# Kernel tuning notes

Hardware: AMD Instinct MI355X
Metric: run time of the kernel (lower is better)

The kernel has to match this reference:

```python
import jax, jax.numpy as jnp
import numpy as np

NEG_SLOPE = 0.2
EPS = 1e-16


def gat_layer(x, src, dst, W, att_src, att_dst, bias, heads, out_ch, concat, n_nodes):
    # Linear projection -> [N, H, C]
    h = (x @ W).reshape(n_nodes, heads, out_ch)
    # Per-node attention logits [N, H]
    a_src = (h * att_src[None]).sum(-1)
    a_dst = (h * att_dst[None]).sum(-1)
    # Per-edge logits, LeakyReLU (message j -> i with src=j, dst=i)
    alpha = a_src[src] + a_dst[dst]                      # [E, H]
    alpha = jnp.where(alpha >= 0, alpha, NEG_SLOPE * alpha)
    # Segment softmax over incoming edges of each dst node
    amax = jax.ops.segment_max(alpha, dst, num_segments=n_nodes)  # [N, H]
    ealpha = jnp.exp(alpha - amax[dst])
    denom = jax.ops.segment_sum(ealpha, dst, num_segments=n_nodes)
    alpha = ealpha / (denom[dst] + EPS)
    # Weighted messages + scatter-add aggregation
    msg = h[src] * alpha[..., None]                      # [E, H, C]
    out = jax.ops.segment_sum(msg, dst, num_segments=n_nodes)  # [N, H, C]
    out = out.reshape(n_nodes, heads * out_ch) if concat else out.mean(axis=1)
    return out + bias


def setup_inputs() -> dict:
    key = jax.random.key(0)
    ks = jax.random.split(key, 11)
    N, E, F, H, C1 = 50000, 1600000, 128, 8, 8
    x = jax.random.normal(ks[0], (N, F), dtype=jnp.float32)
    edge_index = jax.random.randint(ks[1], (2, E), 0, N, dtype=jnp.int64)
    s = 1.0 / np.sqrt(F)
    W1 = jax.random.normal(ks[2], (F, H * C1), dtype=jnp.float32) * s
    att_src1 = jax.random.normal(ks[3], (H, C1), dtype=jnp.float32) * 0.1
    att_dst1 = jax.random.normal(ks[4], (H, C1), dtype=jnp.float32) * 0.1
    bias1 = jax.random.normal(ks[5], (H * C1,), dtype=jnp.float32) * 0.1
    W2 = jax.random.normal(ks[6], (H * C1, F), dtype=jnp.float32) * (1.0 / np.sqrt(H * C1))
    att_src2 = jax.random.normal(ks[7], (1, F), dtype=jnp.float32) * 0.1
    att_dst2 = jax.random.normal(ks[8], (1, F), dtype=jnp.float32) * 0.1
    bias2 = jax.random.normal(ks[9], (F,), dtype=jnp.float32) * 0.1
    return {"x": x, "edge_index": edge_index, "W1": W1, "att_src1": att_src1,
            "att_dst1": att_dst1, "bias1": bias1, "W2": W2, "att_src2": att_src2,
            "att_dst2": att_dst2, "bias2": bias2}


def reference(x, edge_index, W1, att_src1, att_dst1, bias1, W2, att_src2, att_dst2, bias2):
    N = x.shape[0]
    # PyG GATConv add_self_loops=True: append (i, i) for every node
    loops = jnp.arange(N, dtype=edge_index.dtype)
    src = jnp.concatenate([edge_index[0], loops])
    dst = jnp.concatenate([edge_index[1], loops])
    # eval mode: dropouts are identity
    h = gat_layer(x, src, dst, W1, att_src1, att_dst1, bias1, heads=8, out_ch=8,
                  concat=True, n_nodes=N)            # [N, 64]
    h = jax.nn.elu(h)
    out = gat_layer(h, src, dst, W2, att_src2, att_dst2, bias2, heads=1, out_ch=128,
                    concat=False, n_nodes=N)         # [N, 128]
    return out
```

## Files before the change

kernel.cpp:

```cpp
#include <hip/hip_runtime.h>
#include <stdint.h>

#define NEG_SLOPE 0.2f
#define EPSV 1e-16f
#define LOG2E 1.44269504088896340736f
#define NBLK 256

typedef __attribute__((ext_vector_type(8))) _Float16 half8;
typedef __attribute__((ext_vector_type(4))) float f32x4;

__device__ inline void get_edge(const void* ei, int is64, int E, int e, int& s, int& d){
  if (e >= E){ s = d = e - E; return; }
  if (is64){
    const long long* p = (const long long*)ei;
    s = (int)p[e]; d = (int)p[(long long)E + e];
  } else {
    const int* p = (const int*)ei;
    s = p[e]; d = p[E + e];
  }
}

__device__ inline int get_dst(const void* ei, int is64, int E, int e){
  if (e >= E) return e - E;
  if (is64) return (int)((const long long*)ei)[(long long)E + e];
  return ((const int*)ei)[E + e];
}

__device__ inline void pack_one(const float* W, _Float16* Wp, int NCOL, int idx){
  int NNT = NCOL >> 4;
  int j = idx & 7, n16 = (idx >> 3) & 15, q = (idx >> 7) & 3, tile = idx >> 9;
  int nt = tile % NNT, kt = tile / NNT;
  int k = kt*32 + q*8 + j, n = nt*16 + n16;
  Wp[idx] = (_Float16)W[k*NCOL + n];
}
__global__ void prep(const int* __restrict__ ei32, int* __restrict__ flag,
                     const float* __restrict__ W1, _Float16* __restrict__ W1p,
                     const float* __restrict__ W2, _Float16* __restrict__ W2p,
                     const float* __restrict__ as2, const float* __restrict__ ad2,
                     float* __restrict__ va_s, float* __restrict__ va_d){
  int b = blockIdx.x, t = threadIdx.x;
  if (b < 64){
    int idx = b*256 + t;
    if (idx < 8192) pack_one(W1, W1p, 64, idx);
    else            pack_one(W2, W2p, 128, idx - 8192);
  } else {
    if (t == 0){
      int nz = 0;
      for (int i = 0; i < 64; ++i) nz |= ei32[2*i + 1];
      *flag = (nz == 0) ? 1 : 0;
    }
    if (t < 64){
      float s = 0.f, d = 0.f;
      for (int c = 0; c < 128; ++c){
        float w = W2[t*128 + c];
        s = fmaf(w, as2[c], s);
        d = fmaf(w, ad2[c], d);
      }
      va_s[t] = s * LOG2E; va_d[t] = d * LOG2E;
    }
  }
}

__global__ __launch_bounds__(256) void gemm1(const float* __restrict__ x, const _Float16* __restrict__ Bp,
                                             const float* __restrict__ att_s, const float* __restrict__ att_d,
                                             _Float16* __restrict__ Cb,
                                             float* __restrict__ asrc1, float* __restrict__ adst1, int M){
  constexpr int NKT = 4, NNT = 4;
  int wave = (blockIdx.x*256 + (int)threadIdx.x) >> 6;
  int lane = threadIdx.x & 63;
  int row0 = wave << 4;
  if (row0 >= M) return;
  int m = lane & 15, q = lane >> 4;
  f32x4 acc[NNT];
#pragma unroll
  for (int i = 0; i < NNT; ++i) acc[i] = (f32x4){0.f,0.f,0.f,0.f};
#pragma unroll
  for (int kt = 0; kt < NKT; ++kt){
    const float* xr = x + (size_t)(row0 + m)*128 + kt*32 + q*8;
    f32x4 f0 = *(const f32x4*)xr;
    f32x4 f1 = *(const f32x4*)(xr + 4);
    half8 a;
#pragma unroll
    for (int j = 0; j < 4; ++j){ a[j] = (_Float16)f0[j]; a[4 + j] = (_Float16)f1[j]; }
#pragma unroll
    for (int nt = 0; nt < NNT; ++nt){
      half8 b = *(const half8*)(Bp + (size_t)(((kt*NNT + nt)*4 + q)*16 + m)*8);
      acc[nt] = __builtin_amdgcn_mfma_f32_16x16x32_f16(a, b, acc[nt], 0, 0, 0);
    }
  }
#pragma unroll
  for (int nt = 0; nt < NNT; ++nt){
#pragma unroll
    for (int r = 0; r < 4; ++r){
      Cb[(size_t)(row0 + q*4 + r)*64 + nt*16 + m] = (_Float16)acc[nt][r];
    }
  }
  float atts[4], attd[4];
#pragma unroll
  for (int nt = 0; nt < 4; ++nt){
    atts[nt] = att_s[nt*16 + m] * LOG2E;
    attd[nt] = att_d[nt*16 + m] * LOG2E;
  }
  int isw = (m & 7) == 0;
#pragma unroll
  for (int r = 0; r < 4; ++r){
    int row = row0 + q*4 + r;
#pragma unroll
    for (int nt = 0; nt < 4; ++nt){
      float ps = acc[nt][r] * atts[nt];
      float pd = acc[nt][r] * attd[nt];
#pragma unroll
      for (int mm = 1; mm <= 4; mm <<= 1){
        ps += __shfl_xor(ps, mm, 64);
        pd += __shfl_xor(pd, mm, 64);
      }
      if (isw){
        int head = 2*nt + (m >> 3);
        asrc1[row*8 + head] = ps;
        adst1[row*8 + head] = pd;
      }
    }
  }
}

__global__ __launch_bounds__(256) void gemm2(const _Float16* __restrict__ A, const _Float16* __restrict__ Bp,
                                             const float* __restrict__ bias,
                                             float* __restrict__ C, int M){
  constexpr int NKT = 2, NNT = 8;
  int wave = (blockIdx.x*256 + (int)threadIdx.x) >> 6;
  int lane = threadIdx.x & 63;
  int row0 = wave << 4;
  if (row0 >= M) return;
  int m = lane & 15, q = lane >> 4;
  f32x4 acc[NNT];
#pragma unroll
  for (int i = 0; i < NNT; ++i) acc[i] = (f32x4){0.f,0.f,0.f,0.f};
#pragma unroll
  for (int kt = 0; kt < NKT; ++kt){
    half8 a = *(const half8*)(A + (size_t)(row0 + m)*64 + kt*32 + q*8);
#pragma unroll
    for (int nt = 0; nt < NNT; ++nt){
      half8 b = *(const half8*)(Bp + (size_t)(((kt*NNT + nt)*4 + q)*16 + m)*8);
      acc[nt] = __builtin_amdgcn_mfma_f32_16x16x32_f16(a, b, acc[nt], 0, 0, 0);
    }
  }
#pragma unroll
  for (int nt = 0; nt < NNT; ++nt){
    float bv = bias[nt*16 + m];
#pragma unroll
    for (int r = 0; r < 4; ++r){
      C[(size_t)(row0 + q*4 + r)*128 + nt*16 + m] = acc[nt][r] + bv;
    }
  }
}

__global__ __launch_bounds__(256) void p1_hist(const void* ei, const int* flag, int E, int E2,
                                               int* __restrict__ block_counts){
  __shared__ int h[256];
  int t = threadIdx.x, blk = blockIdx.x;
  h[t] = 0; __syncthreads();
  int chunk = (E2 + NBLK - 1)/NBLK;
  int beg = blk*chunk, end = min(beg + chunk, E2);
  int is64 = *flag;
  for (int e = beg + t; e < end; e += 256){
    int d = get_dst(ei, is64, E, e);
    atomicAdd(&h[d >> 8], 1);
  }
  __syncthreads();
  block_counts[blk*256 + t] = h[t];
}

__global__ __launch_bounds__(256) void p2_scan(const int* __restrict__ block_counts,
                                               int* __restrict__ bucket_base,
                                               int* __restrict__ block_off){
  __shared__ int tot[256];
  __shared__ int ex[256];
  __shared__ int col[256];
  int b = blockIdx.x, t = threadIdx.x;
  int s = 0;
  for (int w = 0; w < NBLK; ++w) s += block_counts[w*256 + t];
  tot[t] = s; __syncthreads();
  for (int off = 1; off < 256; off <<= 1){
    int v = (t >= off) ? tot[t - off] : 0;
    __syncthreads(); tot[t] += v; __syncthreads();
  }
  ex[t] = tot[t] - s;
  __syncthreads();
  if (b == 0){
    bucket_base[t] = ex[t];
    if (t == 255) bucket_base[256] = tot[255];
  }
  int base = ex[b];
  int v = block_counts[t*256 + b];
  col[t] = v; __syncthreads();
  for (int off = 1; off < 256; off <<= 1){
    int u = (t >= off) ? col[t - off] : 0;
    __syncthreads(); col[t] += u; __syncthreads();
  }
  block_off[t*256 + b] = base + col[t] - v;
}

__global__ __launch_bounds__(256) void p3_scatter(const void* ei, const int* flag, int E, int E2,
                                                  const int* __restrict__ block_off,
                                                  unsigned* __restrict__ packed){
  __shared__ int cur[256];
  int t = threadIdx.x, blk = blockIdx.x;
  cur[t] = block_off[blk*256 + t];
  __syncthreads();
  int chunk = (E2 + NBLK - 1)/NBLK;
  int beg = blk*chunk, end = min(beg + chunk, E2);
  int is64 = *flag;
  for (int e = beg + t; e < end; e += 256){
    int s, d; get_edge(ei, is64, E, e, s, d);
    int pos = atomicAdd(&cur[d >> 8], 1);
    packed[pos] = ((unsigned)s << 8) | (unsigned)(d & 255);
  }
}

__global__ __launch_bounds__(256) void p4_sort(const unsigned* __restrict__ packed,
                                               const int* __restrict__ bucket_base,
                                               int N, int E2,
                                               int* __restrict__ offs, int* __restrict__ srcs){
  __shared__ int hist[256];
  __shared__ int cur[256];
  int b = blockIdx.x, t = threadIdx.x;
  int base = bucket_base[b], cnt = bucket_base[b + 1] - base;
  hist[t] = 0; __syncthreads();
  for (int p = t; p < cnt; p += 256){
    atomicAdd(&hist[packed[base + p] & 255u], 1);
  }
  __syncthreads();
  int v = hist[t];
  cur[t] = v; __syncthreads();
  for (int off = 1; off < 256; off <<= 1){
    int u = (t >= off) ? cur[t - off] : 0;
    __syncthreads(); cur[t] += u; __syncthreads();
  }
  int ex = cur[t] - v;
  __syncthreads();
  cur[t] = ex;
  int node = b*256 + t;
  if (node < N) offs[node] = base + ex;
  __syncthreads();
  for (int p = t; p < cnt; p += 256){
    unsigned pk = packed[base + p];
    int pos = atomicAdd(&cur[pk & 255u], 1);
    srcs[base + pos] = (int)((pk >> 8) << 7);
  }
  if (b == 0 && t == 0) offs[N] = E2;
}

__global__ __launch_bounds__(256) void agg_l1(const char* __restrict__ h1b,
                       const float* __restrict__ asrc, const float* __restrict__ adst,
                       const int* __restrict__ offs, const int* __restrict__ srcs,
                       const float* __restrict__ bias,
                       const float* __restrict__ va_s, const float* __restrict__ va_d,
                       uint4* __restrict__ hout,
                       float* __restrict__ asrc2, float* __restrict__ adst2, int N){
  int tid = threadIdx.x;
  int i = blockIdx.x*4 + (tid >> 6);
  if (i >= N) return;
  int lane = tid & 63, g = lane >> 3, c = lane & 7;
  unsigned coff = (unsigned)(c << 4);
  float ad = adst[i*8 + c];
  int beg = offs[i], end = offs[i + 1], last = end - 1;
  float acc[8];
#pragma unroll
  for (int k = 0; k < 8; ++k) acc[k] = 0.f;
  float den = 0.f;
  for (int p = beg; p < end; p += 32){
    int m[4]; unsigned so[4];
#pragma unroll
    for (int k = 0; k < 4; ++k) m[k] = p + 8*k + g;
#pragma unroll
    for (int k = 0; k < 4; ++k) so[k] = (unsigned)srcs[min(m[k], last)];
    float a[4];
#pragma unroll
    for (int k = 0; k < 4; ++k) a[k] = asrc[(so[k] >> 4) + (unsigned)c];
    half8 v[4];
#pragma unroll
    for (int k = 0; k < 4; ++k) v[k] = *(const half8*)(h1b + (size_t)(so[k] + coff));
    float w[4];
#pragma unroll
    for (int k = 0; k < 4; ++k){
      float z = a[k] + ad;
      z = fmaxf(z, NEG_SLOPE*z);
      w[k] = (m[k] < end) ? exp2f(z) : 0.f;
      den += w[k];
    }
#pragma unroll
    for (int k = 0; k < 4; ++k){
#pragma unroll
      for (int j = 0; j < 8; ++j){
        acc[j] = fmaf((float)v[k][j], w[k], acc[j]);
      }
    }
  }
#pragma unroll
  for (int mm = 8; mm <= 32; mm <<= 1){
#pragma unroll
    for (int k = 0; k < 8; ++k) acc[k] += __shfl_xor(acc[k], mm, 64);
    den += __shfl_xor(den, mm, 64);
  }
  if (g == 0){
    float inv = 1.f/(den + EPSV);
    float o[8];
    union { _Float16 h[8]; uint4 u; } ov;
#pragma unroll
    for (int k = 0; k < 8; ++k){
      float t = acc[k]*inv + bias[c*8 + k];
      t = (t > 0.f) ? t : (__expf(t) - 1.f);
      o[k] = t;
      ov.h[k] = (_Float16)t;
    }
    hout[(size_t)i*8 + c] = ov.u;
    float ps = 0.f, pd = 0.f;
#pragma unroll
    for (int k = 0; k < 8; ++k){
      ps = fmaf(o[k], va_s[c*8 + k], ps);
      pd = fmaf(o[k], va_d[c*8 + k], pd);
    }
#pragma unroll
    for (int mm = 1; mm <= 4; mm <<= 1){
      ps += __shfl_xor(ps, mm, 8);
      pd += __shfl_xor(pd, mm, 8);
    }
    if (c == 0){ asrc2[i] = ps; adst2[i] = pd; }
  }
}

__global__ __launch_bounds__(256) void agg_l2(const char* __restrict__ hin2,
                       const float* __restrict__ asrc, const float* __restrict__ adst,
                       const int* __restrict__ offs, const int* __restrict__ srcs,
                       uint4* __restrict__ qout, int N){
  int tid = threadIdx.x;
  int i = blockIdx.x*4 + (tid >> 6);
  if (i >= N) return;
  int lane = tid & 63, g = lane >> 3, c = lane & 7;
  unsigned coff = (unsigned)(c << 4);
  float ad = adst[i];
  int beg = offs[i], end = offs[i + 1], last = end - 1;
  float acc[8];
#pragma unroll
  for (int k = 0; k < 8; ++k) acc[k] = 0.f;
  float den = 0.f;
  for (int p = beg; p < end; p += 32){
    int m[4]; unsigned so[4];
#pragma unroll
    for (int k = 0; k < 4; ++k) m[k] = p + 8*k + g;
#pragma unroll
    for (int k = 0; k < 4; ++k) so[k] = (unsigned)srcs[min(m[k], last)];
    float a[4];
#pragma unroll
    for (int k = 0; k < 4; ++k) a[k] = asrc[so[k] >> 7];
    half8 v[4];
#pragma unroll
    for (int k = 0; k < 4; ++k) v[k] = *(const half8*)(hin2 + (size_t)(so[k] + coff));
    float w[4];
#pragma unroll
    for (int k = 0; k < 4; ++k){
      float z = a[k] + ad;
      z = fmaxf(z, NEG_SLOPE*z);
      w[k] = (m[k] < end) ? exp2f(z) : 0.f;
      den += w[k];
    }
#pragma unroll
    for (int k = 0; k < 4; ++k){
#pragma unroll
      for (int j = 0; j < 8; ++j){
        acc[j] = fmaf((float)v[k][j], w[k], acc[j]);
      }
    }
  }
#pragma unroll
  for (int mm = 8; mm <= 32; mm <<= 1){
#pragma unroll
    for (int k = 0; k < 8; ++k) acc[k] += __shfl_xor(acc[k], mm, 64);
    den += __shfl_xor(den, mm, 64);
  }
  if (g == 0){
    float inv = 1.f/(den + EPSV);
    union { _Float16 h[8]; uint4 u; } ov;
#pragma unroll
    for (int k = 0; k < 8; ++k) ov.h[k] = (_Float16)(acc[k]*inv);
    qout[(size_t)i*8 + c] = ov.u;
  }
}

extern "C" void kernel_launch(void* const* d_in, const int* in_sizes, int n_in,
                              void* d_out, int out_size, void* d_ws, size_t ws_size,
                              hipStream_t stream){
  const float* x   = (const float*)d_in[0];
  const void*  ei  = d_in[1];
  const float* W1  = (const float*)d_in[2];
  const float* as1 = (const float*)d_in[3];
  const float* ad1 = (const float*)d_in[4];
  const float* b1  = (const float*)d_in[5];
  const float* W2  = (const float*)d_in[6];
  const float* as2 = (const float*)d_in[7];
  const float* ad2 = (const float*)d_in[8];
  const float* b2  = (const float*)d_in[9];

  int N  = in_sizes[0] / 128;
  int E  = in_sizes[1] / 2;
  int E2 = E + N;
  int NB = (N + 255) >> 8;

  char* p = (char*)d_ws;
  auto alloc = [&](size_t bytes) -> void* {
    void* r = (void*)p;
    p += (bytes + 255) & ~(size_t)255;
    return r;
  };
  _Float16* W1p    = (_Float16*)alloc((size_t)128*64*2);
  _Float16* W2p    = (_Float16*)alloc((size_t)64*128*2);
  _Float16* h1b    = (_Float16*)alloc((size_t)N*64*2);
  float*    asrc1  = (float*)alloc((size_t)N*8*4);
  float*    adst1  = (float*)alloc((size_t)N*8*4);
  _Float16* hin2   = (_Float16*)alloc((size_t)N*64*2);
  _Float16* hq     = (_Float16*)alloc((size_t)N*64*2);
  float*    asrc2  = (float*)alloc((size_t)N*4);
  float*    adst2  = (float*)alloc((size_t)N*4);
  float*    va_s2  = (float*)alloc(64*4);
  float*    va_d2  = (float*)alloc(64*4);
  int*      offs   = (int*)alloc((size_t)(N + 1)*4);
  int*      srcs   = (int*)alloc((size_t)E2*4);
  unsigned* packed = (unsigned*)alloc((size_t)E2*4);
  int*      bcnt   = (int*)alloc((size_t)NBLK*256*4);
  int*      boff   = (int*)alloc((size_t)NBLK*256*4);
  int*      bbase  = (int*)alloc(257*4);
  int*      flag   = (int*)alloc(4);

  dim3 B(256);
  prep<<<65, B, 0, stream>>>((const int*)ei, flag, W1, W1p, W2, W2p, as2, ad2, va_s2, va_d2);

  int nwav = (N + 15)/16;
  gemm1<<<(nwav + 3)/4, B, 0, stream>>>(x, W1p, as1, ad1, h1b, asrc1, adst1, N);

  p1_hist<<<NBLK, B, 0, stream>>>(ei, flag, E, E2, bcnt);
  p2_scan<<<256, B, 0, stream>>>(bcnt, bbase, boff);
  p3_scatter<<<NBLK, B, 0, stream>>>(ei, flag, E, E2, boff, packed);
  p4_sort<<<NB, B, 0, stream>>>(packed, bbase, N, E2, offs, srcs);

  agg_l1<<<(N + 3)/4, B, 0, stream>>>((const char*)h1b, asrc1, adst1, offs, srcs, b1,
                                      va_s2, va_d2, (uint4*)hin2, asrc2, adst2, N);

  agg_l2<<<(N + 3)/4, B, 0, stream>>>((const char*)hin2, asrc2, adst2, offs, srcs,
                                      (uint4*)hq, N);

  gemm2<<<(nwav + 3)/4, B, 0, stream>>>(hq, W2p, b2, (float*)d_out, N);
}
```

Baseline: 237.5 us.

## Split feature channels into two half-width planes to shrink gather working set

```diff
diff --git a/kernel.cpp b/kernel.cpp
--- a/kernel.cpp
+++ b/kernel.cpp
@@ -63,8 +63,9 @@
 
 __global__ __launch_bounds__(256) void gemm1(const float* __restrict__ x, const _Float16* __restrict__ Bp,
                                              const float* __restrict__ att_s, const float* __restrict__ att_d,
-                                             _Float16* __restrict__ Cb,
-                                             float* __restrict__ asrc1, float* __restrict__ adst1, int M){
+                                             _Float16* __restrict__ h1A, _Float16* __restrict__ h1B,
+                                             float* __restrict__ asrc1A, float* __restrict__ adst1A,
+                                             float* __restrict__ asrc1B, float* __restrict__ adst1B, int M){
   constexpr int NKT = 4, NNT = 4;
   int wave = (blockIdx.x*256 + (int)threadIdx.x) >> 6;
   int lane = threadIdx.x & 63;
@@ -90,9 +91,11 @@
   }
 #pragma unroll
   for (int nt = 0; nt < NNT; ++nt){
+    _Float16* hb = (nt < 2) ? h1A : h1B;
+    int ch = (nt & 1)*16 + m;
 #pragma unroll
     for (int r = 0; r < 4; ++r){
-      Cb[(size_t)(row0 + q*4 + r)*64 + nt*16 + m] = (_Float16)acc[nt][r];
+      hb[(size_t)(row0 + q*4 + r)*32 + ch] = (_Float16)acc[nt][r];
     }
   }
   float atts[4], attd[4];
@@ -115,15 +118,18 @@
         pd += __shfl_xor(pd, mm, 64);
       }
       if (isw){
-        int head = 2*nt + (m >> 3);
-        asrc1[row*8 + head] = ps;
-        adst1[row*8 + head] = pd;
+        float* as = (nt < 2) ? asrc1A : asrc1B;
+        float* ap = (nt < 2) ? adst1A : adst1B;
+        int hi = 2*(nt & 1) + (m >> 3);
+        as[row*4 + hi] = ps;
+        ap[row*4 + hi] = pd;
       }
     }
   }
 }
 
-__global__ __launch_bounds__(256) void gemm2(const _Float16* __restrict__ A, const _Float16* __restrict__ Bp,
+__global__ __launch_bounds__(256) void gemm2(const _Float16* __restrict__ hqA, const _Float16* __restrict__ hqB,
+                                             const _Float16* __restrict__ Bp,
                                              const float* __restrict__ bias,
                                              float* __restrict__ C, int M){
   constexpr int NKT = 2, NNT = 8;
@@ -137,7 +143,8 @@
   for (int i = 0; i < NNT; ++i) acc[i] = (f32x4){0.f,0.f,0.f,0.f};
 #pragma unroll
   for (int kt = 0; kt < NKT; ++kt){
-    half8 a = *(const half8*)(A + (size_t)(row0 + m)*64 + kt*32 + q*8);
+    const _Float16* At = (kt == 0) ? hqA : hqB;
+    half8 a = *(const half8*)(At + (size_t)(row0 + m)*32 + q*8);
 #pragma unroll
     for (int nt = 0; nt < NNT; ++nt){
       half8 b = *(const half8*)(Bp + (size_t)(((kt*NNT + nt)*4 + q)*16 + m)*8);
@@ -245,59 +252,52 @@
   for (int p = t; p < cnt; p += 256){
     unsigned pk = packed[base + p];
     int pos = atomicAdd(&cur[pk & 255u], 1);
-    srcs[base + pos] = (int)((pk >> 8) << 7);
+    srcs[base + pos] = (int)((pk >> 8) << 6);
   }
   if (b == 0 && t == 0) offs[N] = E2;
 }
 
-__global__ __launch_bounds__(256) void agg_l1(const char* __restrict__ h1b,
-                       const float* __restrict__ asrc, const float* __restrict__ adst,
+template<int P>
+__global__ __launch_bounds__(256) void agg1(const char* __restrict__ hP,
+                       const char* __restrict__ asrcP, const float* __restrict__ adstP,
                        const int* __restrict__ offs, const int* __restrict__ srcs,
                        const float* __restrict__ bias,
                        const float* __restrict__ va_s, const float* __restrict__ va_d,
-                       uint4* __restrict__ hout,
+                       uint4* __restrict__ houtP,
+                       float* __restrict__ psA, float* __restrict__ pdA,
                        float* __restrict__ asrc2, float* __restrict__ adst2, int N){
   int tid = threadIdx.x;
   int i = blockIdx.x*4 + (tid >> 6);
   if (i >= N) return;
-  int lane = tid & 63, g = lane >> 3, c = lane & 7;
+  int lane = tid & 63, g = lane >> 2, c = lane & 3;
   unsigned coff = (unsigned)(c << 4);
-  float ad = adst[i*8 + c];
+  float ad = adstP[i*4 + c];
   int beg = offs[i], end = offs[i + 1], last = end - 1;
   float acc[8];
 #pragma unroll
   for (int k = 0; k < 8; ++k) acc[k] = 0.f;
   float den = 0.f;
   for (int p = beg; p < end; p += 32){
-    int m[4]; unsigned so[4];
-#pragma unroll
-    for (int k = 0; k < 4; ++k) m[k] = p + 8*k + g;
-#pragma unroll
-    for (int k = 0; k < 4; ++k) so[k] = (unsigned)srcs[min(m[k], last)];
-    float a[4];
-#pragma unroll
-    for (int k = 0; k < 4; ++k) a[k] = asrc[(so[k] >> 4) + (unsigned)c];
-    half8 v[4];
-#pragma unroll
-    for (int k = 0; k < 4; ++k) v[k] = *(const half8*)(h1b + (size_t)(so[k] + coff));
-    float w[4];
-#pragma unroll
-    for (int k = 0; k < 4; ++k){
-      float z = a[k] + ad;
-      z = fmaxf(z, NEG_SLOPE*z);
-      w[k] = (m[k] < end) ? exp2f(z) : 0.f;
-      den += w[k];
-    }
-#pragma unroll
-    for (int k = 0; k < 4; ++k){
-#pragma unroll
-      for (int j = 0; j < 8; ++j){
-        acc[j] = fmaf((float)v[k][j], w[k], acc[j]);
-      }
-    }
-  }
-#pragma unroll
-  for (int mm = 8; mm <= 32; mm <<= 1){
+    int m0 = p + g, m1 = p + 16 + g;
+    unsigned s0 = (unsigned)srcs[min(m0, last)];
+    unsigned s1 = (unsigned)srcs[min(m1, last)];
+    float a0 = *(const float*)(asrcP + (s0 >> 2) + (c << 2));
+    float a1 = *(const float*)(asrcP + (s1 >> 2) + (c << 2));
+    half8 v0 = *(const half8*)(hP + (size_t)(s0 + coff));
+    half8 v1 = *(const half8*)(hP + (size_t)(s1 + coff));
+    float z0 = a0 + ad; z0 = fmaxf(z0, NEG_SLOPE*z0);
+    float z1 = a1 + ad; z1 = fmaxf(z1, NEG_SLOPE*z1);
+    float w0 = (m0 < end) ? exp2f(z0) : 0.f;
+    float w1 = (m1 < end) ? exp2f(z1) : 0.f;
+    den += w0 + w1;
+#pragma unroll
+    for (int j = 0; j < 8; ++j){
+      acc[j] = fmaf((float)v0[j], w0, acc[j]);
+      acc[j] = fmaf((float)v1[j], w1, acc[j]);
+    }
+  }
+#pragma unroll
+  for (int mm = 4; mm <= 32; mm <<= 1){
 #pragma unroll
     for (int k = 0; k < 8; ++k) acc[k] += __shfl_xor(acc[k], mm, 64);
     den += __shfl_xor(den, mm, 64);
@@ -308,72 +308,63 @@
     union { _Float16 h[8]; uint4 u; } ov;
 #pragma unroll
     for (int k = 0; k < 8; ++k){
-      float t = acc[k]*inv + bias[c*8 + k];
+      float t = acc[k]*inv + bias[P*32 + c*8 + k];
       t = (t > 0.f) ? t : (__expf(t) - 1.f);
       o[k] = t;
       ov.h[k] = (_Float16)t;
     }
-    hout[(size_t)i*8 + c] = ov.u;
+    houtP[(size_t)i*4 + c] = ov.u;
     float ps = 0.f, pd = 0.f;
 #pragma unroll
     for (int k = 0; k < 8; ++k){
-      ps = fmaf(o[k], va_s[c*8 + k], ps);
-      pd = fmaf(o[k], va_d[c*8 + k], pd);
-    }
-#pragma unroll
-    for (int mm = 1; mm <= 4; mm <<= 1){
-      ps += __shfl_xor(ps, mm, 8);
-      pd += __shfl_xor(pd, mm, 8);
-    }
-    if (c == 0){ asrc2[i] = ps; adst2[i] = pd; }
-  }
-}
-
-__global__ __launch_bounds__(256) void agg_l2(const char* __restrict__ hin2,
-                       const float* __restrict__ asrc, const float* __restrict__ adst,
+      ps = fmaf(o[k], va_s[P*32 + c*8 + k], ps);
+      pd = fmaf(o[k], va_d[P*32 + c*8 + k], pd);
+    }
+    ps += __shfl_xor(ps, 1, 64); ps += __shfl_xor(ps, 2, 64);
+    pd += __shfl_xor(pd, 1, 64); pd += __shfl_xor(pd, 2, 64);
+    if (c == 0){
+      if (P == 0){ psA[i] = ps; pdA[i] = pd; }
+      else       { asrc2[i] = psA[i] + ps; adst2[i] = pdA[i] + pd; }
+    }
+  }
+}
+
+__global__ __launch_bounds__(256) void agg2(const char* __restrict__ hinP,
+                       const char* __restrict__ as2b, const float* __restrict__ adst2,
                        const int* __restrict__ offs, const int* __restrict__ srcs,
-                       uint4* __restrict__ qout, int N){
+                       uint4* __restrict__ qoutP, int N){
   int tid = threadIdx.x;
   int i = blockIdx.x*4 + (tid >> 6);
   if (i >= N) return;
-  int lane = tid & 63, g = lane >> 3, c = lane & 7;
+  int lane = tid & 63, g = lane >> 2, c = lane & 3;
   unsigned coff = (unsigned)(c << 4);
-  float ad = adst[i];
+  float ad = adst2[i];
   int beg = offs[i], end = offs[i + 1], last = end - 1;
   float acc[8];
 #pragma unroll
   for (int k = 0; k < 8; ++k) acc[k] = 0.f;
   float den = 0.f;
   for (int p = beg; p < end; p += 32){
-    int m[4]; unsigned so[4];
-#pragma unroll
-    for (int k = 0; k < 4; ++k) m[k] = p + 8*k + g;
-#pragma unroll
-    for (int k = 0; k < 4; ++k) so[k] = (unsigned)srcs[min(m[k], last)];
-    float a[4];
-#pragma unroll
-    for (int k = 0; k < 4; ++k) a[k] = asrc[so[k] >> 7];
-    half8 v[4];
-#pragma unroll
-    for (int k = 0; k < 4; ++k) v[k] = *(const half8*)(hin2 + (size_t)(so[k] + coff));
-    float w[4];
-#pragma unroll
-    for (int k = 0; k < 4; ++k){
-      float z = a[k] + ad;
-      z = fmaxf(z, NEG_SLOPE*z);
-      w[k] = (m[k] < end) ? exp2f(z) : 0.f;
-      den += w[k];
-    }
-#pragma unroll
-    for (int k = 0; k < 4; ++k){
-#pragma unroll
-      for (int j = 0; j < 8; ++j){
-        acc[j] = fmaf((float)v[k][j], w[k], acc[j]);
-      }
-    }
-  }
-#pragma unroll
-  for (int mm = 8; mm <= 32; mm <<= 1){
+    int m0 = p + g, m1 = p + 16 + g;
+    unsigned s0 = (unsigned)srcs[min(m0, last)];
+    unsigned s1 = (unsigned)srcs[min(m1, last)];
+    float a0 = *(const float*)(as2b + (s0 >> 4));
+    float a1 = *(const float*)(as2b + (s1 >> 4));
+    half8 v0 = *(const half8*)(hinP + (size_t)(s0 + coff));
+    half8 v1 = *(const half8*)(hinP + (size_t)(s1 + coff));
+    float z0 = a0 + ad; z0 = fmaxf(z0, NEG_SLOPE*z0);
+    float z1 = a1 + ad; z1 = fmaxf(z1, NEG_SLOPE*z1);
+    float w0 = (m0 < end) ? exp2f(z0) : 0.f;
+    float w1 = (m1 < end) ? exp2f(z1) : 0.f;
+    den += w0 + w1;
+#pragma unroll
+    for (int j = 0; j < 8; ++j){
+      acc[j] = fmaf((float)v0[j], w0, acc[j]);
+      acc[j] = fmaf((float)v1[j], w1, acc[j]);
+    }
+  }
+#pragma unroll
+  for (int mm = 4; mm <= 32; mm <<= 1){
 #pragma unroll
     for (int k = 0; k < 8; ++k) acc[k] += __shfl_xor(acc[k], mm, 64);
     den += __shfl_xor(den, mm, 64);
@@ -383,7 +374,7 @@
     union { _Float16 h[8]; uint4 u; } ov;
 #pragma unroll
     for (int k = 0; k < 8; ++k) ov.h[k] = (_Float16)(acc[k]*inv);
-    qout[(size_t)i*8 + c] = ov.u;
+    qoutP[(size_t)i*4 + c] = ov.u;
   }
 }
 
@@ -414,11 +405,18 @@
   };
   _Float16* W1p    = (_Float16*)alloc((size_t)128*64*2);
   _Float16* W2p    = (_Float16*)alloc((size_t)64*128*2);
-  _Float16* h1b    = (_Float16*)alloc((size_t)N*64*2);
-  float*    asrc1  = (float*)alloc((size_t)N*8*4);
-  float*    adst1  = (float*)alloc((size_t)N*8*4);
-  _Float16* hin2   = (_Float16*)alloc((size_t)N*64*2);
-  _Float16* hq     = (_Float16*)alloc((size_t)N*64*2);
+  _Float16* h1A    = (_Float16*)alloc((size_t)N*32*2);
+  _Float16* h1B    = (_Float16*)alloc((size_t)N*32*2);
+  float*    asrc1A = (float*)alloc((size_t)N*4*4);
+  float*    adst1A = (float*)alloc((size_t)N*4*4);
+  float*    asrc1B = (float*)alloc((size_t)N*4*4);
+  float*    adst1B = (float*)alloc((size_t)N*4*4);
+  _Float16* hinA   = (_Float16*)alloc((size_t)N*32*2);
+  _Float16* hinB   = (_Float16*)alloc((size_t)N*32*2);
+  _Float16* hqA    = (_Float16*)alloc((size_t)N*32*2);
+  _Float16* hqB    = (_Float16*)alloc((size_t)N*32*2);
+  float*    psA    = (float*)alloc((size_t)N*4);
+  float*    pdA    = (float*)alloc((size_t)N*4);
   float*    asrc2  = (float*)alloc((size_t)N*4);
   float*    adst2  = (float*)alloc((size_t)N*4);
   float*    va_s2  = (float*)alloc(64*4);
@@ -435,18 +433,26 @@
   prep<<<65, B, 0, stream>>>((const int*)ei, flag, W1, W1p, W2, W2p, as2, ad2, va_s2, va_d2);
 
   int nwav = (N + 15)/16;
-  gemm1<<<(nwav + 3)/4, B, 0, stream>>>(x, W1p, as1, ad1, h1b, asrc1, adst1, N);
+  gemm1<<<(nwav + 3)/4, B, 0, stream>>>(x, W1p, as1, ad1, h1A, h1B,
+                                        asrc1A, adst1A, asrc1B, adst1B, N);
 
   p1_hist<<<NBLK, B, 0, stream>>>(ei, flag, E, E2, bcnt);
   p2_scan<<<256, B, 0, stream>>>(bcnt, bbase, boff);
   p3_scatter<<<NBLK, B, 0, stream>>>(ei, flag, E, E2, boff, packed);
   p4_sort<<<NB, B, 0, stream>>>(packed, bbase, N, E2, offs, srcs);
 
-  agg_l1<<<(N + 3)/4, B, 0, stream>>>((const char*)h1b, asrc1, adst1, offs, srcs, b1,
-                                      va_s2, va_d2, (uint4*)hin2, asrc2, adst2, N);
-
-  agg_l2<<<(N + 3)/4, B, 0, stream>>>((const char*)hin2, asrc2, adst2, offs, srcs,
-                                      (uint4*)hq, N);
-
-  gemm2<<<(nwav + 3)/4, B, 0, stream>>>(hq, W2p, b2, (float*)d_out, N);
-}
+  int gagg = (N + 3)/4;
+  agg1<0><<<gagg, B, 0, stream>>>((const char*)h1A, (const char*)asrc1A, adst1A,
+                                  offs, srcs, b1, va_s2, va_d2,
+                                  (uint4*)hinA, psA, pdA, asrc2, adst2, N);
+  agg1<1><<<gagg, B, 0, stream>>>((const char*)h1B, (const char*)asrc1B, adst1B,
+                                  offs, srcs, b1, va_s2, va_d2,
+                                  (uint4*)hinB, psA, pdA, asrc2, adst2, N);
+
+  agg2<<<gagg, B, 0, stream>>>((const char*)hinA, (const char*)asrc2, adst2,
+                               offs, srcs, (uint4*)hqA, N);
+  agg2<<<gagg, B, 0, stream>>>((const char*)hinB, (const char*)asrc2, adst2,
+                               offs, srcs, (uint4*)hqB, N);
+
+  gemm2<<<(nwav + 3)/4, B, 0, stream>>>(hqA, hqB, W2p, b2, (float*)d_out, N);
+}
```

After: 288.2 us. 21.3% more time.

## Fuse CSR bucketing into prep kernel with atomic fixed-capacity buckets

Applied to the files above, without the earlier changes.

```diff
diff --git a/kernel.cpp b/kernel.cpp
--- a/kernel.cpp
+++ b/kernel.cpp
@@ -5,6 +5,8 @@
 #define EPSV 1e-16f
 #define LOG2E 1.44269504088896340736f
 #define NBLK 256
+#define BCAP 12288
+#define PKCAP 8192
 
 typedef __attribute__((ext_vector_type(8))) _Float16 half8;
 typedef __attribute__((ext_vector_type(4))) float f32x4;
@@ -20,12 +22,6 @@
   }
 }
 
-__device__ inline int get_dst(const void* ei, int is64, int E, int e){
-  if (e >= E) return e - E;
-  if (is64) return (int)((const long long*)ei)[(long long)E + e];
-  return ((const int*)ei)[E + e];
-}
-
 __device__ inline void pack_one(const float* W, _Float16* Wp, int NCOL, int idx){
   int NNT = NCOL >> 4;
   int j = idx & 7, n16 = (idx >> 3) & 15, q = (idx >> 7) & 3, tile = idx >> 9;
@@ -33,22 +29,26 @@
   int k = kt*32 + q*8 + j, n = nt*16 + n16;
   Wp[idx] = (_Float16)W[k*NCOL + n];
 }
-__global__ void prep(const int* __restrict__ ei32, int* __restrict__ flag,
+
+__global__ __launch_bounds__(256) void k1(const void* ei,
                      const float* __restrict__ W1, _Float16* __restrict__ W1p,
                      const float* __restrict__ W2, _Float16* __restrict__ W2p,
                      const float* __restrict__ as2, const float* __restrict__ ad2,
-                     float* __restrict__ va_s, float* __restrict__ va_d){
+                     float* __restrict__ va_s, float* __restrict__ va_d,
+                     int E, int E2,
+                     int* __restrict__ gcnt,
+                     unsigned* __restrict__ packed){
+  __shared__ unsigned pk[PKCAP];
+  __shared__ int h[256];
+  __shared__ int cur[256];
   int b = blockIdx.x, t = threadIdx.x;
   if (b < 64){
     int idx = b*256 + t;
     if (idx < 8192) pack_one(W1, W1p, 64, idx);
     else            pack_one(W2, W2p, 128, idx - 8192);
-  } else {
-    if (t == 0){
-      int nz = 0;
-      for (int i = 0; i < 64; ++i) nz |= ei32[2*i + 1];
-      *flag = (nz == 0) ? 1 : 0;
-    }
+    return;
+  }
+  if (b == 64){
     if (t < 64){
       float s = 0.f, d = 0.f;
       for (int c = 0; c < 128; ++c){
@@ -58,6 +58,33 @@
       }
       va_s[t] = s * LOG2E; va_d[t] = d * LOG2E;
     }
+    return;
+  }
+  int blk = b - 65;
+  int chunk = (E2 + NBLK - 1)/NBLK;
+  int beg = blk*chunk, end = min(beg + chunk, E2), cnt = end - beg;
+  const int* e32 = (const int*)ei;
+  int nz = 0;
+  for (int i = 0; i < 64; ++i) nz |= e32[2*i + 1];
+  int is64 = (nz == 0) ? 1 : 0;
+  h[t] = 0; __syncthreads();
+  for (int j = t; j < cnt; j += 256){
+    int s, d; get_edge(ei, is64, E, beg + j, s, d);
+    unsigned p = ((unsigned)s << 16) | (unsigned)d;
+    pk[j] = p;
+    atomicAdd(&h[(p >> 8) & 255u], 1);
+  }
+  __syncthreads();
+  int mine = h[t];
+  int base_t = 0;
+  if (mine > 0) base_t = atomicAdd(&gcnt[t*16], mine);
+  cur[t] = base_t;
+  __syncthreads();
+  for (int j = t; j < cnt; j += 256){
+    unsigned p = pk[j];
+    int bk = (p >> 8) & 255u;
+    int pos = atomicAdd(&cur[bk], 1);
+    packed[(size_t)bk*BCAP + pos] = p;
   }
 }
 
@@ -154,80 +181,28 @@
   }
 }
 
-__global__ __launch_bounds__(256) void p1_hist(const void* ei, const int* flag, int E, int E2,
-                                               int* __restrict__ block_counts){
-  __shared__ int h[256];
-  int t = threadIdx.x, blk = blockIdx.x;
-  h[t] = 0; __syncthreads();
-  int chunk = (E2 + NBLK - 1)/NBLK;
-  int beg = blk*chunk, end = min(beg + chunk, E2);
-  int is64 = *flag;
-  for (int e = beg + t; e < end; e += 256){
-    int d = get_dst(ei, is64, E, e);
-    atomicAdd(&h[d >> 8], 1);
-  }
-  __syncthreads();
-  block_counts[blk*256 + t] = h[t];
-}
-
-__global__ __launch_bounds__(256) void p2_scan(const int* __restrict__ block_counts,
-                                               int* __restrict__ bucket_base,
-                                               int* __restrict__ block_off){
-  __shared__ int tot[256];
-  __shared__ int ex[256];
-  __shared__ int col[256];
-  int b = blockIdx.x, t = threadIdx.x;
-  int s = 0;
-  for (int w = 0; w < NBLK; ++w) s += block_counts[w*256 + t];
-  tot[t] = s; __syncthreads();
-  for (int off = 1; off < 256; off <<= 1){
-    int v = (t >= off) ? tot[t - off] : 0;
-    __syncthreads(); tot[t] += v; __syncthreads();
-  }
-  ex[t] = tot[t] - s;
-  __syncthreads();
-  if (b == 0){
-    bucket_base[t] = ex[t];
-    if (t == 255) bucket_base[256] = tot[255];
-  }
-  int base = ex[b];
-  int v = block_counts[t*256 + b];
-  col[t] = v; __syncthreads();
-  for (int off = 1; off < 256; off <<= 1){
-    int u = (t >= off) ? col[t - off] : 0;
-    __syncthreads(); col[t] += u; __syncthreads();
-  }
-  block_off[t*256 + b] = base + col[t] - v;
-}
-
-__global__ __launch_bounds__(256) void p3_scatter(const void* ei, const int* flag, int E, int E2,
-                                                  const int* __restrict__ block_off,
-                                                  unsigned* __restrict__ packed){
-  __shared__ int cur[256];
-  int t = threadIdx.x, blk = blockIdx.x;
-  cur[t] = block_off[blk*256 + t];
-  __syncthreads();
-  int chunk = (E2 + NBLK - 1)/NBLK;
-  int beg = blk*chunk, end = min(beg + chunk, E2);
-  int is64 = *flag;
-  for (int e = beg + t; e < end; e += 256){
-    int s, d; get_edge(ei, is64, E, e, s, d);
-    int pos = atomicAdd(&cur[d >> 8], 1);
-    packed[pos] = ((unsigned)s << 8) | (unsigned)(d & 255);
-  }
-}
-
 __global__ __launch_bounds__(256) void p4_sort(const unsigned* __restrict__ packed,
-                                               const int* __restrict__ bucket_base,
+                                               const int* __restrict__ gcnt,
                                                int N, int E2,
                                                int* __restrict__ offs, int* __restrict__ srcs){
   __shared__ int hist[256];
   __shared__ int cur[256];
+  __shared__ int tot[256];
+  __shared__ int sbase, scnt;
   int b = blockIdx.x, t = threadIdx.x;
-  int base = bucket_base[b], cnt = bucket_base[b + 1] - base;
+  int v0 = gcnt[t*16];
+  tot[t] = v0; __syncthreads();
+  for (int off = 1; off < 256; off <<= 1){
+    int v = (t >= off) ? tot[t - off] : 0;
+    __syncthreads(); tot[t] += v; __syncthreads();
+  }
+  if (t == b){ sbase = tot[t] - v0; scnt = v0; }
+  __syncthreads();
+  int base = sbase, cnt = scnt;
   hist[t] = 0; __syncthreads();
+  const unsigned* bp = packed + (size_t)b*BCAP;
   for (int p = t; p < cnt; p += 256){
-    atomicAdd(&hist[packed[base + p] & 255u], 1);
+    atomicAdd(&hist[bp[p] & 255u], 1);
   }
   __syncthreads();
   int v = hist[t];
@@ -243,9 +218,9 @@
   if (node < N) offs[node] = base + ex;
   __syncthreads();
   for (int p = t; p < cnt; p += 256){
-    unsigned pk = packed[base + p];
+    unsigned pk = bp[p];
     int pos = atomicAdd(&cur[pk & 255u], 1);
-    srcs[base + pos] = (int)((pk >> 8) << 7);
+    srcs[base + pos] = (int)((pk >> 16) << 7);
   }
   if (b == 0 && t == 0) offs[N] = E2;
 }
@@ -425,22 +400,19 @@
   float*    va_d2  = (float*)alloc(64*4);
   int*      offs   = (int*)alloc((size_t)(N + 1)*4);
   int*      srcs   = (int*)alloc((size_t)E2*4);
-  unsigned* packed = (unsigned*)alloc((size_t)E2*4);
-  int*      bcnt   = (int*)alloc((size_t)NBLK*256*4);
-  int*      boff   = (int*)alloc((size_t)NBLK*256*4);
-  int*      bbase  = (int*)alloc(257*4);
-  int*      flag   = (int*)alloc(4);
+  unsigned* packed = (unsigned*)alloc((size_t)256*BCAP*4);
+  int*      gcnt   = (int*)alloc((size_t)256*16*4);
 
   dim3 B(256);
-  prep<<<65, B, 0, stream>>>((const int*)ei, flag, W1, W1p, W2, W2p, as2, ad2, va_s2, va_d2);
+  hipMemsetAsync(gcnt, 0, (size_t)256*16*4, stream);
+
+  k1<<<65 + NBLK, B, 0, stream>>>(ei, W1, W1p, W2, W2p, as2, ad2, va_s2, va_d2,
+                                  E, E2, gcnt, packed);
 
   int nwav = (N + 15)/16;
   gemm1<<<(nwav + 3)/4, B, 0, stream>>>(x, W1p, as1, ad1, h1b, asrc1, adst1, N);
 
-  p1_hist<<<NBLK, B, 0, stream>>>(ei, flag, E, E2, bcnt);
-  p2_scan<<<256, B, 0, stream>>>(bcnt, bbase, boff);
-  p3_scatter<<<NBLK, B, 0, stream>>>(ei, flag, E, E2, boff, packed);
-  p4_sort<<<NB, B, 0, stream>>>(packed, bbase, N, E2, offs, srcs);
+  p4_sort<<<NB, B, 0, stream>>>(packed, gcnt, N, E2, offs, srcs);
 
   agg_l1<<<(N + 3)/4, B, 0, stream>>>((const char*)h1b, asrc1, adst1, offs, srcs, b1,
                                       va_s2, va_d2, (uint4*)hin2, asrc2, adst2, N);
```

After: 223.6 us. 5.8% less time.
